# Kernel optimization log

Measured on AMD Instinct MI355X. Metric: run time of the kernel, lower is better.

## Reference

```python
import jax, jax.numpy as jnp
import numpy as np

B, C, H = 8, 512, 2048
GROUPS = 32
EPS = 1e-6


def setup_inputs() -> dict:
    key = jax.random.key(0)
    ks = jax.random.split(key, 10)
    s = 1.0 / np.sqrt(C)
    return {
        "x": jax.random.normal(ks[0], (B, C, H), dtype=jnp.float32),
        "gamma": jnp.ones((C,), jnp.float32),
        "beta": jnp.zeros((C,), jnp.float32),
        "wq": jax.random.normal(ks[1], (C, C), jnp.float32) * s,
        "bq": jnp.zeros((C,), jnp.float32),
        "wk": jax.random.normal(ks[2], (C, C), jnp.float32) * s,
        "bk": jnp.zeros((C,), jnp.float32),
        "wv": jax.random.normal(ks[3], (C, C), jnp.float32) * s,
        "bv": jnp.zeros((C,), jnp.float32),
        "wp": jax.random.normal(ks[4], (C, C), jnp.float32) * s,
        "bp": jnp.zeros((C,), jnp.float32),
    }


def group_norm(x, gamma, beta):
    b, c, h = x.shape
    xr = x.reshape(b, GROUPS, c // GROUPS, h)
    mean = xr.mean(axis=(2, 3), keepdims=True)
    var = xr.var(axis=(2, 3), keepdims=True)
    xn = ((xr - mean) * jax.lax.rsqrt(var + EPS)).reshape(b, c, h)
    return xn * gamma[None, :, None] + beta[None, :, None]


def conv1x1(x, w, b):
    # 1x1 Conv1d == channel-mixing GEMM: [C_out,C_in] x [b,C_in,h]
    return jnp.einsum("oc,bch->boh", w, x) + b[None, :, None]


def reference(x, gamma, beta, wq, bq, wk, bk, wv, bv, wp, bp):
    b, c, h = x.shape
    hn = group_norm(x, gamma, beta)
    q = conv1x1(hn, wq, bq)  # [b,c,h]
    k = conv1x1(hn, wk, bk)
    v = conv1x1(hn, wv, bv)
    # scores w[b,i,j] = sum_c q[b,c,i] k[b,c,j] / sqrt(c)
    w = jnp.einsum("bci,bcj->bij", q, k) * (c ** -0.5)
    w = jax.nn.softmax(w, axis=2)
    # h_[b,c,i] = sum_j v[b,c,j] w[b,i,j]
    h_ = jnp.einsum("bcj,bij->bci", v, w)
    out = conv1x1(h_, wp, bp)
    return x + out
```

## Files before the change

### kernel.cpp

```cpp
#include <hip/hip_runtime.h>
#include <stdint.h>

typedef unsigned short u16;
typedef short s16x8 __attribute__((ext_vector_type(8)));
typedef float f32x4 __attribute__((ext_vector_type(4)));

#define BM 128
#define BN 128
#define BK 32
#define KPAD 40

#define WAITV(n) asm volatile("s_waitcnt vmcnt(" #n ")" ::: "memory")
#define BARR()   asm volatile("s_barrier" ::: "memory")
#define SB0()    __builtin_amdgcn_sched_barrier(0)

__device__ __forceinline__ float bf2f(u16 b) {
    union { unsigned int u; float f; } v; v.u = ((unsigned int)b) << 16; return v.f;
}
__device__ __forceinline__ u16 f2bf(float f) {
    union { float f; unsigned int u; } v; v.f = f;
    unsigned int u = v.u;
    u += 0x7fffu + ((u >> 16) & 1u);
    return (u16)(u >> 16);
}
__device__ __forceinline__ void async_cp16(const u16* g, u16* l) {
    __builtin_amdgcn_global_load_lds((const __attribute__((address_space(1))) void*)g,
                                     (__attribute__((address_space(3))) void*)l, 16, 0, 0);
}

__global__ __launch_bounds__(256) void gn_stats(const float* __restrict__ x,
                                                float* __restrict__ mean,
                                                float* __restrict__ rstd) {
    const int bg = blockIdx.x;
    const float* p = x + (long)bg * 16 * 2048;
    float s = 0.f, ss = 0.f;
    for (int it = 0; it < 32; it++) {
        const float4 v = *reinterpret_cast<const float4*>(p + ((it * 256 + threadIdx.x) << 2));
        s += v.x + v.y + v.z + v.w;
        ss += v.x * v.x + v.y * v.y + v.z * v.z + v.w * v.w;
    }
    const int lane = threadIdx.x & 63, wave = threadIdx.x >> 6;
#pragma unroll
    for (int o = 32; o > 0; o >>= 1) { s += __shfl_down(s, o, 64); ss += __shfl_down(ss, o, 64); }
    __shared__ float rb[8];
    if (lane == 0) { rb[wave] = s; rb[4 + wave] = ss; }
    __syncthreads();
    if (threadIdx.x == 0) {
        float S = rb[0] + rb[1] + rb[2] + rb[3];
        float SS = rb[4] + rb[5] + rb[6] + rb[7];
        float mu = S * (1.f / 32768.f);
        float var = SS * (1.f / 32768.f) - mu * mu;
        mean[bg] = mu;
        rstd[bg] = rsqrtf(var + 1e-6f);
    }
}

__global__ __launch_bounds__(256) void gn_apply_t(const float* __restrict__ x,
                                                  const float* __restrict__ gamma,
                                                  const float* __restrict__ beta,
                                                  const float* __restrict__ mean,
                                                  const float* __restrict__ rstd,
                                                  u16* __restrict__ hnT) {
    const int b = blockIdx.z, c0 = blockIdx.y * 64, h0 = blockIdx.x * 64;
    __shared__ __align__(16) u16 T[64][72];
    const int tid = threadIdx.x;
#pragma unroll
    for (int sidx = 0; sidx < 4; sidx++) {
        int ch = tid + sidx * 256;
        int cc = ch >> 4, h4 = (ch & 15) * 4;
        int c = c0 + cc;
        float mu = mean[b * 32 + (c >> 4)], rs = rstd[b * 32 + (c >> 4)];
        float ga = gamma[c], be = beta[c];
        const float4 v = *reinterpret_cast<const float4*>(x + ((long)b * 512 + c) * 2048 + h0 + h4);
        ushort4 pk;
        pk.x = f2bf((v.x - mu) * rs * ga + be);
        pk.y = f2bf((v.y - mu) * rs * ga + be);
        pk.z = f2bf((v.z - mu) * rs * ga + be);
        pk.w = f2bf((v.w - mu) * rs * ga + be);
        *reinterpret_cast<ushort4*>(&T[cc][h4]) = pk;
    }
    __syncthreads();
#pragma unroll
    for (int sidx = 0; sidx < 2; sidx++) {
        int ch = tid + sidx * 256;
        int hh = ch >> 3, c8 = (ch & 7) * 8;
        unsigned int o[4];
#pragma unroll
        for (int i = 0; i < 4; i++) {
            u16 lo = T[c8 + 2 * i][hh];
            u16 hi = T[c8 + 2 * i + 1][hh];
            o[i] = (unsigned int)lo | ((unsigned int)hi << 16);
        }
        *reinterpret_cast<uint4*>(hnT + ((long)b * 2048 + h0 + hh) * 512 + c0 + c8) =
            uint4{o[0], o[1], o[2], o[3]};
    }
}

__global__ __launch_bounds__(256) void w2bf(const float* __restrict__ a,
                                            const float* __restrict__ b,
                                            const float* __restrict__ c,
                                            u16* __restrict__ dst) {
    const float* s = (blockIdx.y == 0) ? a : (blockIdx.y == 1) ? b : c;
    const int i = (blockIdx.x * 256 + threadIdx.x) * 4;
    const float4 v = *reinterpret_cast<const float4*>(s + i);
    ushort4 p;
    p.x = f2bf(v.x); p.y = f2bf(v.y); p.z = f2bf(v.z); p.w = f2bf(v.w);
    *reinterpret_cast<ushort4*>(dst + (long)blockIdx.y * 262144 + i) = p;
}

__global__ __launch_bounds__(256) void softmax_rows(u16* __restrict__ S) {
    u16* p = S + (long)blockIdx.x * 2048;
    const int tid = threadIdx.x;
    uint4 v = *reinterpret_cast<const uint4*>(p + (tid << 3));
    unsigned int w[4] = {v.x, v.y, v.z, v.w};
    float f[8];
#pragma unroll
    for (int i = 0; i < 4; i++) {
        f[2 * i]     = bf2f((u16)(w[i] & 0xffffu));
        f[2 * i + 1] = bf2f((u16)(w[i] >> 16));
    }
    float m = f[0];
#pragma unroll
    for (int i = 1; i < 8; i++) m = fmaxf(m, f[i]);
    const int lane = tid & 63, wave = tid >> 6;
#pragma unroll
    for (int o = 32; o > 0; o >>= 1) m = fmaxf(m, __shfl_down(m, o, 64));
    __shared__ float rb[4];
    __shared__ float bc;
    if (lane == 0) rb[wave] = m;
    __syncthreads();
    if (tid == 0) bc = fmaxf(fmaxf(rb[0], rb[1]), fmaxf(rb[2], rb[3]));
    __syncthreads();
    m = bc;
    float s = 0.f;
#pragma unroll
    for (int i = 0; i < 8; i++) { f[i] = __expf(f[i] - m); s += f[i]; }
#pragma unroll
    for (int o = 32; o > 0; o >>= 1) s += __shfl_down(s, o, 64);
    __syncthreads();
    if (lane == 0) rb[wave] = s;
    __syncthreads();
    if (tid == 0) bc = 1.f / (rb[0] + rb[1] + rb[2] + rb[3]);
    __syncthreads();
    const float inv = bc;
#pragma unroll
    for (int i = 0; i < 4; i++)
        w[i] = (unsigned int)f2bf(f[2 * i] * inv) | ((unsigned int)f2bf(f[2 * i + 1] * inv) << 16);
    *reinterpret_cast<uint4*>(p + (tid << 3)) = uint4{w[0], w[1], w[2], w[3]};
}

__global__ __launch_bounds__(512, 1) void gemm256_s(const u16* __restrict__ Ag, long sA,
                                                    const u16* __restrict__ Bg, long sB,
                                                    u16* __restrict__ Og, long sO,
                                                    int K, int lda, int ldb, int ldo,
                                                    float scale) {
    const int bx = blockIdx.x;
    const int b = bx & 7, s = bx >> 3;
    const int ty = s & 7, tx = s >> 3;
    const int m0 = ty * 256, n0 = tx * 256;
    Ag += (long)b * sA;
    Bg += (long)b * sB;
    u16* O = Og + (long)b * sO;

    __shared__ __align__(16) u16 LA[2][2][128 * 64];
    __shared__ __align__(16) u16 LB[2][2][128 * 64];

    const int tid = threadIdx.x;
    const int lane = tid & 63, wave = tid >> 6;
    const int wm = wave >> 2, w4 = wave & 3;
    const int l15 = lane & 15, quad = lane >> 4;

    const int qxu   = ((quad << 4) ^ ((lane & 4) << 3)) >> 1;
    const int arow_u = (wm * 64 + l15) * 64;
    const int brow_u = (w4 * 32 + l15) * 64;

    const int l8 = lane >> 3;
    const int lrow0 = wave * 8 + l8;
    const int sEl = (((lane & 7) ^ ((lane & 32) >> 4)) << 3);
    int pA[2], pB[2];
    pA[0] = (m0 + lrow0) * lda + sEl;
    pA[1] = (m0 + 64 + lrow0) * lda + sEl;
    {
        const int gb = (lrow0 >> 5) * 64 + (lrow0 & 31);
        pB[0] = (n0 + gb) * ldb + sEl;
        pB[1] = (n0 + gb + 32) * ldb + sEl;
    }
    const int jA = 128 * lda;
    const int jB = 128 * ldb;

    auto stageA = [&](int buf, int mh, int k0) {
        u16* d = &LA[buf][mh][wave * 512];
        async_cp16(Ag + pA[mh] + k0, d);
        async_cp16(Ag + pA[mh] + jA + k0, d + 4096);
    };
    auto stageB = [&](int buf, int nh, int k0) {
        u16* d = &LB[buf][nh][wave * 512];
        async_cp16(Bg + pB[nh] + k0, d);
        async_cp16(Bg + pB[nh] + jB + k0, d + 4096);
    };

    f32x4 acc[8][4];
#pragma unroll
    for (int i = 0; i < 8; i++)
#pragma unroll
        for (int j = 0; j < 4; j++) acc[i][j] = f32x4{0.f, 0.f, 0.f, 0.f};

    s16x8 fa[4][2], fblo[2][2], fbhi[2][2];

    const int NT = K >> 6;

    stageA(0, 0, 0);
    stageB(0, 0, 0);
    stageB(0, 1, 0);
    stageA(0, 1, 0);
    if (NT > 1) {
        stageA(1, 0, 64);
        stageB(1, 0, 64);
        stageB(1, 1, 64);
    }
    WAITV(8); SB0();
    BARR(); SB0();

    for (int t = 0; t < NT; t++) {
        const int buf = t & 1;
        const int k2 = (t + 2) << 6;
        {
            const u16* Ar = &LA[buf][0][0];
            const u16* Br = &LB[buf][0][0];
#pragma unroll
            for (int mf = 0; mf < 4; mf++)
#pragma unroll
                for (int ks = 0; ks < 2; ks++)
                    fa[mf][ks] = *reinterpret_cast<const s16x8*>(Ar + arow_u + mf * 1024 + ks * 32 + qxu);
#pragma unroll
            for (int nf = 0; nf < 2; nf++)
#pragma unroll
                for (int ks = 0; ks < 2; ks++)
                    fblo[nf][ks] = *reinterpret_cast<const s16x8*>(Br + brow_u + nf * 1024 + ks * 32 + qxu);
            if (t + 1 < NT) stageA(buf ^ 1, 1, (t + 1) << 6);
            if (t == NT - 1) { WAITV(2); } else { WAITV(8); }
            SB0();
            BARR(); SB0();
            __builtin_amdgcn_s_setprio(1);
#pragma unroll
            for (int mf = 0; mf < 4; mf++)
#pragma unroll
                for (int nf = 0; nf < 2; nf++)
#pragma unroll
                    for (int ks = 0; ks < 2; ks++)
                        acc[mf][nf] = __builtin_amdgcn_mfma_f32_16x16x32_bf16(fa[mf][ks], fblo[nf][ks], acc[mf][nf], 0, 0, 0);
            __builtin_amdgcn_s_setprio(0);
            BARR(); SB0();
        }
        {
            const u16* Br = &LB[buf][1][0];
#pragma unroll
            for (int nf = 0; nf < 2; nf++)
#pragma unroll
                for (int ks = 0; ks < 2; ks++)
                    fbhi[nf][ks] = *reinterpret_cast<const s16x8*>(Br + brow_u + nf * 1024 + ks * 32 + qxu);
            if (t + 2 < NT) stageA(buf, 0, k2);
            if (t == NT - 1) { WAITV(0); } else { WAITV(8); }
            SB0();
            BARR(); SB0();
            __builtin_amdgcn_s_setprio(1);
#pragma unroll
            for (int mf = 0; mf < 4; mf++)
#pragma unroll
                for (int nf = 0; nf < 2; nf++)
#pragma unroll
                    for (int ks = 0; ks < 2; ks++)
                        acc[mf][2 + nf] = __builtin_amdgcn_mfma_f32_16x16x32_bf16(fa[mf][ks], fbhi[nf][ks], acc[mf][2 + nf], 0, 0, 0);
            __builtin_amdgcn_s_setprio(0);
            BARR(); SB0();
        }
        {
            const u16* Ar = &LA[buf][1][0];
#pragma unroll
            for (int mf = 0; mf < 4; mf++)
#pragma unroll
                for (int ks = 0; ks < 2; ks++)
                    fa[mf][ks] = *reinterpret_cast<const s16x8*>(Ar + arow_u + mf * 1024 + ks * 32 + qxu);
            if (t + 2 < NT) stageB(buf, 0, k2);
            WAITV(8); SB0();
            BARR(); SB0();
            __builtin_amdgcn_s_setprio(1);
#pragma unroll
            for (int mf = 0; mf < 4; mf++)
#pragma unroll
                for (int nf = 0; nf < 2; nf++)
#pragma unroll
                    for (int ks = 0; ks < 2; ks++)
                        acc[4 + mf][2 + nf] = __builtin_amdgcn_mfma_f32_16x16x32_bf16(fa[mf][ks], fbhi[nf][ks], acc[4 + mf][2 + nf], 0, 0, 0);
            __builtin_amdgcn_s_setprio(0);
            BARR(); SB0();
        }
        {
            if (t + 2 < NT) stageB(buf, 1, k2);
            if (t == NT - 2) { WAITV(4); } else { WAITV(8); }
            SB0();
            BARR(); SB0();
            __builtin_amdgcn_s_setprio(1);
#pragma unroll
            for (int mf = 0; mf < 4; mf++)
#pragma unroll
                for (int nf = 0; nf < 2; nf++)
#pragma unroll
                    for (int ks = 0; ks < 2; ks++)
                        acc[4 + mf][nf] = __builtin_amdgcn_mfma_f32_16x16x32_bf16(fa[mf][ks], fblo[nf][ks], acc[4 + mf][nf], 0, 0, 0);
            __builtin_amdgcn_s_setprio(0);
            BARR(); SB0();
        }
    }

    const int orow = m0 + wm * 128 + quad * 4;
    const int ocol = n0 + w4 * 64 + l15;
#pragma unroll
    for (int mi = 0; mi < 8; mi++)
#pragma unroll
        for (int ni = 0; ni < 4; ni++) {
            const long rb = (long)(orow + mi * 16) * ldo + ocol + ni * 16;
#pragma unroll
            for (int r = 0; r < 4; r++)
                O[rb + (long)r * ldo] = f2bf(acc[mi][ni][r] * scale);
        }
}

template <int EPI, int SWIZ>
__global__ __launch_bounds__(256) void gemm_tn_a(const u16* __restrict__ Ag, long sA,
                                                 const u16* __restrict__ Bg, long sB,
                                                 const float* __restrict__ bias,
                                                 const float* __restrict__ Xg, long sX,
                                                 void* __restrict__ Ogv, long sO,
                                                 int K, int lda, int ldb, int ldo,
                                                 float scale) {
    const int b = blockIdx.z;
    Ag += (long)b * sA;
    Bg += (long)b * sB;
    int tx, ty;
    if (SWIZ == 1) {
        const int xcd = blockIdx.x & 7, s = blockIdx.x >> 3;
        ty = xcd + 8 * (s >> 2);
        tx = s & 3;
    } else if (SWIZ == 2) {
        const int xcd = blockIdx.x & 7, s = blockIdx.x >> 3;
        ty = (xcd & 3) * 4 + (s & 3);
        tx = (xcd >> 2) * 8 + (s >> 2);
    } else {
        tx = blockIdx.x; ty = blockIdx.y;
    }
    const int m0 = ty * BM;
    const int n0 = tx * BN;

    __shared__ __align__(16) u16 As[3][BM * BK];
    __shared__ __align__(16) u16 Bs[3][BN * BK];

    const int tid = threadIdx.x;
    const int wave = tid >> 6;
    const int lane = tid & 63;
    const int quad = lane >> 4;
    const int l16 = lane & 15;
    const int wm = (wave >> 1) * 64;
    const int wn = (wave & 1) * 64;
    const int rl = lane >> 2;
    const int cl = (lane & 3) * 8;

    f32x4 acc[4][4];
#pragma unroll
    for (int i = 0; i < 4; i++)
#pragma unroll
        for (int j = 0; j < 4; j++) acc[i][j] = f32x4{0.f, 0.f, 0.f, 0.f};

    auto stage = [&](int buf, int k0) {
#pragma unroll
        for (int j = 0; j < 2; j++) {
            const int rbase = wave * 32 + j * 16;
            async_cp16(Ag + (long)(m0 + rbase + rl) * lda + k0 + cl, &As[buf][rbase * BK]);
            async_cp16(Bg + (long)(n0 + rbase + rl) * ldb + k0 + cl, &Bs[buf][rbase * BK]);
        }
    };
    auto compute = [&](int buf) {
        s16x8 af[4], bfr[4];
#pragma unroll
        for (int i = 0; i < 4; i++)
            af[i] = *reinterpret_cast<const s16x8*>(&As[buf][(wm + i * 16 + l16) * BK + quad * 8]);
#pragma unroll
        for (int j = 0; j < 4; j++)
            bfr[j] = *reinterpret_cast<const s16x8*>(&Bs[buf][(wn + j * 16 + l16) * BK + quad * 8]);
#pragma unroll
        for (int i = 0; i < 4; i++)
#pragma unroll
            for (int j = 0; j < 4; j++)
                acc[i][j] = __builtin_amdgcn_mfma_f32_16x16x32_bf16(af[i], bfr[j], acc[i][j], 0, 0, 0);
    };

    const int nsteps = K / BK;
    stage(0, 0);
    stage(1, BK);
    int t = 0;
    for (; t < nsteps - 1; t++) {
        asm volatile("s_waitcnt vmcnt(4)" ::: "memory");
        asm volatile("s_barrier" ::: "memory");
        if (t + 2 < nsteps) stage((t + 2) % 3, (t + 2) * BK);
        compute(t % 3);
    }
    asm volatile("s_waitcnt vmcnt(0)" ::: "memory");
    asm volatile("s_barrier" ::: "memory");
    compute(t % 3);

#pragma unroll
    for (int i = 0; i < 4; i++) {
        const int mb = m0 + wm + i * 16 + quad * 4;
#pragma unroll
        for (int j = 0; j < 4; j++) {
            const int n = n0 + wn + j * 16 + l16;
            if (EPI == 0) {
                u16* O = (u16*)Ogv + (long)b * sO;
#pragma unroll
                for (int r = 0; r < 4; r++) {
                    float vv = acc[i][j][r] * scale;
                    if (bias) vv += bias[mb + r];
                    O[(long)(mb + r) * ldo + n] = f2bf(vv);
                }
            } else if (EPI == 1) {
                u16* O = (u16*)Ogv + (long)b * sO;
                ushort4 pk;
                pk.x = f2bf(acc[i][j][0] + bias[mb + 0]);
                pk.y = f2bf(acc[i][j][1] + bias[mb + 1]);
                pk.z = f2bf(acc[i][j][2] + bias[mb + 2]);
                pk.w = f2bf(acc[i][j][3] + bias[mb + 3]);
                *reinterpret_cast<ushort4*>(&O[(long)n * ldo + mb]) = pk;
            } else {
                float* O = (float*)Ogv + (long)b * sO;
                const float* X = Xg + (long)b * sX;
                const float bn = bias[n];
                const float4 xv = *reinterpret_cast<const float4*>(&X[(long)n * ldo + mb]);
                float4 pk;
                pk.x = acc[i][j][0] + bn + xv.x;
                pk.y = acc[i][j][1] + bn + xv.y;
                pk.z = acc[i][j][2] + bn + xv.z;
                pk.w = acc[i][j][3] + bn + xv.w;
                *reinterpret_cast<float4*>(&O[(long)n * ldo + mb]) = pk;
            }
        }
    }
}

__global__ __launch_bounds__(256) void qkv_a(const u16* __restrict__ wb3,
                                             const u16* __restrict__ hnT,
                                             const float* __restrict__ bq,
                                             const float* __restrict__ bk,
                                             const float* __restrict__ bv,
                                             u16* __restrict__ qT, u16* __restrict__ kT,
                                             u16* __restrict__ vv) {
    const long HC = 1048576;
    const int b = blockIdx.z;
    const int xcd = blockIdx.x & 7, s = blockIdx.x >> 3;
    const int hi = (s >= 12) ? 1 : 0;
    const int yy = s - hi * 12;
    const int x = xcd + 8 * hi;
    const int which = yy >> 2;
    const int my = yy & 3;
    const u16* Ag = wb3 + which * 262144;
    const u16* Bg = hnT + (long)b * HC;
    const int m0 = my * BM;
    const int n0 = x * BN;

    __shared__ __align__(16) u16 As[3][BM * BK];
    __shared__ __align__(16) u16 Bs[3][BN * BK];

    const int tid = threadIdx.x;
    const int wave = tid >> 6;
    const int lane = tid & 63;
    const int quad = lane >> 4;
    const int l16 = lane & 15;
    const int wm = (wave >> 1) * 64;
    const int wn = (wave & 1) * 64;
    const int rl = lane >> 2;
    const int cl = (lane & 3) * 8;

    f32x4 acc[4][4];
#pragma unroll
    for (int i = 0; i < 4; i++)
#pragma unroll
        for (int j = 0; j < 4; j++) acc[i][j] = f32x4{0.f, 0.f, 0.f, 0.f};

    auto stage = [&](int buf, int k0) {
#pragma unroll
        for (int j = 0; j < 2; j++) {
            const int rbase = wave * 32 + j * 16;
            async_cp16(Ag + (long)(m0 + rbase + rl) * 512 + k0 + cl, &As[buf][rbase * BK]);
            async_cp16(Bg + (long)(n0 + rbase + rl) * 512 + k0 + cl, &Bs[buf][rbase * BK]);
        }
    };
    auto compute = [&](int buf) {
        s16x8 af[4], bfr[4];
#pragma unroll
        for (int i = 0; i < 4; i++)
            af[i] = *reinterpret_cast<const s16x8*>(&As[buf][(wm + i * 16 + l16) * BK + quad * 8]);
#pragma unroll
        for (int j = 0; j < 4; j++)
            bfr[j] = *reinterpret_cast<const s16x8*>(&Bs[buf][(wn + j * 16 + l16) * BK + quad * 8]);
#pragma unroll
        for (int i = 0; i < 4; i++)
#pragma unroll
            for (int j = 0; j < 4; j++)
                acc[i][j] = __builtin_amdgcn_mfma_f32_16x16x32_bf16(af[i], bfr[j], acc[i][j], 0, 0, 0);
    };

    const int nsteps = 512 / BK;
    stage(0, 0);
    stage(1, BK);
    int t = 0;
    for (; t < nsteps - 1; t++) {
        asm volatile("s_waitcnt vmcnt(4)" ::: "memory");
        asm volatile("s_barrier" ::: "memory");
        if (t + 2 < nsteps) stage((t + 2) % 3, (t + 2) * BK);
        compute(t % 3);
    }
    asm volatile("s_waitcnt vmcnt(0)" ::: "memory");
    asm volatile("s_barrier" ::: "memory");
    compute(t % 3);

    if (which == 2) {
        u16* O = vv + (long)b * HC;
#pragma unroll
        for (int i = 0; i < 4; i++) {
            const int mb = m0 + wm + i * 16 + quad * 4;
#pragma unroll
            for (int j = 0; j < 4; j++) {
                const int n = n0 + wn + j * 16 + l16;
#pragma unroll
                for (int r = 0; r < 4; r++)
                    O[(long)(mb + r) * 2048 + n] = f2bf(acc[i][j][r] + bv[mb + r]);
            }
        }
    } else {
        const float* bias = which ? bk : bq;
        u16* O = (which ? kT : qT) + (long)b * HC;
#pragma unroll
        for (int i = 0; i < 4; i++) {
            const int mb = m0 + wm + i * 16 + quad * 4;
#pragma unroll
            for (int j = 0; j < 4; j++) {
                const int n = n0 + wn + j * 16 + l16;
                ushort4 pk;
                pk.x = f2bf(acc[i][j][0] + bias[mb + 0]);
                pk.y = f2bf(acc[i][j][1] + bias[mb + 1]);
                pk.z = f2bf(acc[i][j][2] + bias[mb + 2]);
                pk.w = f2bf(acc[i][j][3] + bias[mb + 3]);
                *reinterpret_cast<ushort4*>(&O[(long)n * 512 + mb]) = pk;
            }
        }
    }
}

template <int F32>
__device__ __forceinline__ void stage_tile(const char* G, int ld, int r0, int k0,
                                           u16* __restrict__ lds, int tid) {
    if (F32) {
        const float* g = (const float*)G;
#pragma unroll
        for (int s = 0; s < 4; s++) {
            const int c = tid + s * 256;
            const int row = c >> 3, col = (c & 7) * 4;
            const float4 v = *reinterpret_cast<const float4*>(g + (long)(r0 + row) * ld + k0 + col);
            ushort4 pk;
            pk.x = f2bf(v.x); pk.y = f2bf(v.y); pk.z = f2bf(v.z); pk.w = f2bf(v.w);
            *reinterpret_cast<ushort4*>(&lds[row * KPAD + col]) = pk;
        }
    } else {
        const u16* g = (const u16*)G;
#pragma unroll
        for (int s = 0; s < 2; s++) {
            const int c = tid + s * 256;
            const int row = c >> 2, col = (c & 3) * 8;
            const uint4 v = *reinterpret_cast<const uint4*>(g + (long)(r0 + row) * ld + k0 + col);
            *reinterpret_cast<uint4*>(&lds[row * KPAD + col]) = v;
        }
    }
}

template <int EPI, int AF32, int BF32>
__global__ __launch_bounds__(256) void gemm_tn(const void* __restrict__ Agv, long sA,
                                               const void* __restrict__ Bgv, long sB,
                                               const float* __restrict__ bias,
                                               const float* __restrict__ Xg, long sX,
                                               void* __restrict__ Ogv, long sO,
                                               int K, int lda, int ldb, int ldo,
                                               float scale) {
    const int b = blockIdx.z;
    const char* A8 = (const char*)Agv + (long)b * sA * (AF32 ? 4 : 2);
    const char* B8 = (const char*)Bgv + (long)b * sB * (BF32 ? 4 : 2);
    const int m0 = blockIdx.y * BM;
    const int n0 = blockIdx.x * BN;

    __shared__ __align__(16) u16 As[BM * KPAD];
    __shared__ __align__(16) u16 Bs[BN * KPAD];

    const int tid = threadIdx.x;
    const int wave = tid >> 6;
    const int lane = tid & 63;
    const int quad = lane >> 4;
    const int l16 = lane & 15;
    const int wm = (wave >> 1) * 64;
    const int wn = (wave & 1) * 64;

    f32x4 acc[4][4];
#pragma unroll
    for (int i = 0; i < 4; i++)
#pragma unroll
        for (int j = 0; j < 4; j++) acc[i][j] = f32x4{0.f, 0.f, 0.f, 0.f};

    for (int k0 = 0; k0 < K; k0 += BK) {
        __syncthreads();
        stage_tile<AF32>(A8, lda, m0, k0, As, tid);
        stage_tile<BF32>(B8, ldb, n0, k0, Bs, tid);
        __syncthreads();
        s16x8 af[4], bfr[4];
#pragma unroll
        for (int i = 0; i < 4; i++)
            af[i] = *reinterpret_cast<const s16x8*>(&As[(wm + i * 16 + l16) * KPAD + quad * 8]);
#pragma unroll
        for (int j = 0; j < 4; j++)
            bfr[j] = *reinterpret_cast<const s16x8*>(&Bs[(wn + j * 16 + l16) * KPAD + quad * 8]);
#pragma unroll
        for (int i = 0; i < 4; i++)
#pragma unroll
            for (int j = 0; j < 4; j++)
                acc[i][j] = __builtin_amdgcn_mfma_f32_16x16x32_bf16(af[i], bfr[j], acc[i][j], 0, 0, 0);
    }

#pragma unroll
    for (int i = 0; i < 4; i++) {
        const int mb = m0 + wm + i * 16 + quad * 4;
#pragma unroll
        for (int j = 0; j < 4; j++) {
            const int n = n0 + wn + j * 16 + l16;
            if (EPI == 0) {
                u16* O = (u16*)Ogv + (long)b * sO;
#pragma unroll
                for (int r = 0; r < 4; r++) {
                    float vv = acc[i][j][r] * scale;
                    if (bias) vv += bias[mb + r];
                    O[(long)(mb + r) * ldo + n] = f2bf(vv);
                }
            } else if (EPI == 1) {
                u16* O = (u16*)Ogv + (long)b * sO;
                ushort4 pk;
                pk.x = f2bf(acc[i][j][0] + bias[mb + 0]);
                pk.y = f2bf(acc[i][j][1] + bias[mb + 1]);
                pk.z = f2bf(acc[i][j][2] + bias[mb + 2]);
                pk.w = f2bf(acc[i][j][3] + bias[mb + 3]);
                *reinterpret_cast<ushort4*>(&O[(long)n * ldo + mb]) = pk;
            } else {
                float* O = (float*)Ogv + (long)b * sO;
                const float* X = Xg + (long)b * sX;
                const float bn = bias[n];
                const float4 xv = *reinterpret_cast<const float4*>(&X[(long)n * ldo + mb]);
                float4 pk;
                pk.x = acc[i][j][0] + bn + xv.x;
                pk.y = acc[i][j][1] + bn + xv.y;
                pk.z = acc[i][j][2] + bn + xv.z;
                pk.w = acc[i][j][3] + bn + xv.w;
                *reinterpret_cast<float4*>(&O[(long)n * ldo + mb]) = pk;
            }
        }
    }
}

extern "C" void kernel_launch(void* const* d_in, const int* in_sizes, int n_in,
                              void* d_out, int out_size, void* d_ws, size_t ws_size,
                              hipStream_t stream) {
    const float* x     = (const float*)d_in[0];
    const float* gamma = (const float*)d_in[1];
    const float* beta  = (const float*)d_in[2];
    const float* wq    = (const float*)d_in[3];
    const float* bq    = (const float*)d_in[4];
    const float* wk    = (const float*)d_in[5];
    const float* bk    = (const float*)d_in[6];
    const float* wv    = (const float*)d_in[7];
    const float* bv    = (const float*)d_in[8];
    const float* wp    = (const float*)d_in[9];
    const float* bp    = (const float*)d_in[10];
    float* out = (float*)d_out;

    const long HC = (long)2048 * 512;
    const long HH = (long)2048 * 2048;
    const long WSZ = 512 * 512;
    const float scl = 0.044194173824159216f;

    char* ws = (char*)d_ws;
    float* meanb = (float*)ws;
    float* rstdb = (float*)(ws + 1024);
    u16* base = (u16*)(ws + 4096);

    const size_t FULL_NEED   = 4096 + 2 * (size_t)(24 * HC + 8 * HH);
    const size_t MED_NEED    = 4096 + 2 * (size_t)(32 * HC + HH);
    const size_t SMALL_NEED  = 4096 + 2 * (size_t)(4 * HC + HH);
    const size_t CHUNK512    = 4096 + 2 * (size_t)(4 * HC + 512 * 2048);

    gn_stats<<<256, 256, 0, stream>>>(x, meanb, rstdb);

    if (ws_size >= FULL_NEED) {
        u16* qT  = base;
        u16* kT  = qT + 8 * HC;
        u16* vv  = kT + 8 * HC;
        u16* Sb  = vv + 8 * HC;
        u16* hnT = Sb;
        u16* wb3 = Sb + 8 * HH - 3 * WSZ;
        u16* hT  = qT;
        u16* wpb = vv;

        w2bf<<<dim3(256, 3), 256, 0, stream>>>(wq, wk, wv, wb3);
        gn_apply_t<<<dim3(32, 8, 8), 256, 0, stream>>>(x, gamma, beta, meanb, rstdb, hnT);
        qkv_a<<<dim3(192, 1, 8), 256, 0, stream>>>(wb3, hnT, bq, bk, bv, qT, kT, vv);
        gemm256_s<<<dim3(512), 512, 0, stream>>>(qT, HC, kT, HC, Sb, HH,
                                                 512, 512, 512, 2048, scl);
        softmax_rows<<<16384, 256, 0, stream>>>(Sb);
        gemm_tn_a<0, 1><<<dim3(64, 1, 8), 256, 0, stream>>>(Sb, HH, vv, HC, nullptr, nullptr, 0,
                                                            hT, HC, 2048, 2048, 2048, 512, 1.f);
        w2bf<<<dim3(256, 1), 256, 0, stream>>>(wp, wp, wp, wpb);
        gemm_tn_a<2, 1><<<dim3(64, 1, 8), 256, 0, stream>>>(hT, HC, wpb, 0, bp, x, HC,
                                                            out, HC, 512, 512, 512, 2048, 1.f);
    } else if (ws_size >= MED_NEED) {
        u16* hnT = base;
        u16* qT  = hnT + 8 * HC;
        u16* kT  = qT + 8 * HC;
        u16* vv  = kT + 8 * HC;
        u16* Sb  = vv + 8 * HC;
        u16* hT  = hnT;
        gn_apply_t<<<dim3(32, 8, 8), 256, 0, stream>>>(x, gamma, beta, meanb, rstdb, hnT);
        gemm_tn<1, 1, 0><<<dim3(16, 4, 8), 256, 0, stream>>>(wq, 0, hnT, HC, bq, nullptr, 0,
                                                             qT, HC, 512, 512, 512, 512, 1.f);
        gemm_tn<1, 1, 0><<<dim3(16, 4, 8), 256, 0, stream>>>(wk, 0, hnT, HC, bk, nullptr, 0,
                                                             kT, HC, 512, 512, 512, 512, 1.f);
        gemm_tn<0, 1, 0><<<dim3(16, 4, 8), 256, 0, stream>>>(wv, 0, hnT, HC, bv, nullptr, 0,
                                                             vv, HC, 512, 512, 512, 2048, 1.f);
        for (int b = 0; b < 8; b++) {
            gemm_tn<0, 0, 0><<<dim3(16, 16, 1), 256, 0, stream>>>(qT + b * HC, 0, kT + b * HC, 0,
                                                                  nullptr, nullptr, 0, Sb, 0,
                                                                  512, 512, 512, 2048, scl);
            softmax_rows<<<2048, 256, 0, stream>>>(Sb);
            gemm_tn<0, 0, 0><<<dim3(4, 16, 1), 256, 0, stream>>>(Sb, 0, vv + b * HC, 0,
                                                                 nullptr, nullptr, 0, hT + b * HC, 0,
                                                                 2048, 2048, 2048, 512, 1.f);
        }
        gemm_tn<2, 0, 1><<<dim3(4, 16, 8), 256, 0, stream>>>(hT, HC, wp, 0, bp, x, HC,
                                                             out, HC, 512, 512, 512, 2048, 1.f);
    } else {
        const int CH = (ws_size >= SMALL_NEED) ? 2048 : ((ws_size >= CHUNK512) ? 512 : 128);
        u16* hn = base;
        u16* q  = hn + HC;
        u16* k  = q + HC;
        u16* v  = k + HC;
        u16* Sc = v + HC;
        u16* hT = hn;
        for (int b = 0; b < 8; b++) {
            const float* xb = x + (long)b * HC;
            gn_apply_t<<<dim3(32, 8, 1), 256, 0, stream>>>(xb, gamma, beta,
                                                           meanb + b * 32, rstdb + b * 32, hn);
            gemm_tn<1, 1, 0><<<dim3(16, 4, 1), 256, 0, stream>>>(wq, 0, hn, 0, bq, nullptr, 0,
                                                                 q, 0, 512, 512, 512, 512, 1.f);
            gemm_tn<1, 1, 0><<<dim3(16, 4, 1), 256, 0, stream>>>(wk, 0, hn, 0, bk, nullptr, 0,
                                                                 k, 0, 512, 512, 512, 512, 1.f);
            gemm_tn<0, 1, 0><<<dim3(16, 4, 1), 256, 0, stream>>>(wv, 0, hn, 0, bv, nullptr, 0,
                                                                 v, 0, 512, 512, 512, 2048, 1.f);
            for (int i0 = 0; i0 < 2048; i0 += CH) {
                gemm_tn<0, 0, 0><<<dim3(16, CH / 128, 1), 256, 0, stream>>>(
                    q + (long)i0 * 512, 0, k, 0, nullptr, nullptr, 0, Sc, 0,
                    512, 512, 512, 2048, scl);
                softmax_rows<<<CH, 256, 0, stream>>>(Sc);
                gemm_tn<0, 0, 0><<<dim3(4, CH / 128, 1), 256, 0, stream>>>(
                    Sc, 0, v, 0, nullptr, nullptr, 0, hT + (long)i0 * 512, 0,
                    2048, 2048, 2048, 512, 1.f);
            }
            gemm_tn<2, 0, 1><<<dim3(4, 16, 1), 256, 0, stream>>>(hT, 0, wp, 0, bp, xb, 0,
                                                                 out + (long)b * HC, 0,
                                                                 512, 512, 512, 2048, 1.f);
        }
    }
}
```

Baseline: 302.1 us.

## Add dedicated 256x128 pipelined GEMM kernel for attention-times-V product

Replaces the generic gemm_tn_a launch for the P·V product with a new 512-thread kernel using 256x128 output tiles, double-buffered LDS with async copies split into four compute phases, and swizzled LDS reads. The grid becomes 256 blocks over batch, 8 M tiles and 4 N tiles. The goal is better MFMA utilisation and load/compute overlap on the K=2048 reduction, though fewer blocks than CUs may leave some compute units idle.

```diff
diff --git a/kernel.cpp b/kernel.cpp
--- a/kernel.cpp
+++ b/kernel.cpp
@@ -317,6 +317,167 @@
     const int ocol = n0 + w4 * 64 + l15;
 #pragma unroll
     for (int mi = 0; mi < 8; mi++)
+#pragma unroll
+        for (int ni = 0; ni < 4; ni++) {
+            const long rb = (long)(orow + mi * 16) * ldo + ocol + ni * 16;
+#pragma unroll
+            for (int r = 0; r < 4; r++)
+                O[rb + (long)r * ldo] = f2bf(acc[mi][ni][r] * scale);
+        }
+}
+
+template <int EPI>
+__global__ __launch_bounds__(512, 1) void gemm256_pv(const u16* __restrict__ Ag, long sA,
+                                                     const u16* __restrict__ Bg, long sB,
+                                                     u16* __restrict__ Og, long sO,
+                                                     int K, int lda, int ldb, int ldo,
+                                                     float scale) {
+    const int bx = blockIdx.x;
+    const int b = bx & 7, s = bx >> 3;
+    const int mt = s >> 2, nt = s & 3;
+    const int m0 = mt * 256, n0 = nt * 128;
+    Ag += (long)b * sA;
+    Bg += (long)b * sB;
+    u16* O = Og + (long)b * sO;
+
+    __shared__ __align__(16) u16 LA[2][2][128 * 64];
+    __shared__ __align__(16) u16 LB[2][2][64 * 64];
+
+    const int tid = threadIdx.x;
+    const int lane = tid & 63, wave = tid >> 6;
+    const int wm = wave >> 1, wn = wave & 1;
+    const int l15 = lane & 15, quad = lane >> 4;
+
+    const int qxu = ((quad << 4) ^ ((lane & 4) << 3)) >> 1;
+
+    const int r0 = tid >> 3;
+    const int sEl = (((lane & 7) ^ ((lane & 32) >> 4)) << 3);
+    const int gA = (r0 >> 5) * 64 + (r0 & 31);
+    int pA[2], pB[2];
+    pA[0] = (m0 + gA) * lda + sEl;
+    pA[1] = (m0 + gA + 32) * lda + sEl;
+    pB[0] = (n0 + gA) * ldb + sEl;
+    pB[1] = (n0 + gA + 32) * ldb + sEl;
+    const int jA = 128 * lda;
+
+    auto stageA = [&](int buf, int mh, int k0) {
+        u16* d = &LA[buf][mh][wave * 512];
+        async_cp16(Ag + pA[mh] + k0, d);
+        async_cp16(Ag + pA[mh] + jA + k0, d + 4096);
+    };
+    auto stageBB = [&](int buf, int k0) {
+        async_cp16(Bg + pB[0] + k0, &LB[buf][0][wave * 512]);
+        async_cp16(Bg + pB[1] + k0, &LB[buf][1][wave * 512]);
+    };
+
+    f32x4 acc[4][4];
+#pragma unroll
+    for (int i = 0; i < 4; i++)
+#pragma unroll
+        for (int j = 0; j < 4; j++) acc[i][j] = f32x4{0.f, 0.f, 0.f, 0.f};
+
+    s16x8 fa[2][2], fblo[2][2], fbhi[2][2];
+
+    const int arow_u = (wm * 32 + l15) * 64;
+    const int brow_u = (wn * 32 + l15) * 64;
+
+    const int NT = K >> 6;
+
+    stageBB(0, 0);
+    stageA(0, 0, 0);
+    stageA(0, 1, 0);
+    if (NT > 1) stageBB(1, 64);
+    WAITV(4); SB0();
+    BARR(); SB0();
+
+    for (int t = 0; t < NT; t++) {
+        const int buf = t & 1;
+        const int k1 = (t + 1) << 6, k2 = (t + 2) << 6;
+        {
+            const u16* Ar = &LA[buf][0][0];
+            const u16* Br = &LB[buf][0][0];
+#pragma unroll
+            for (int mf = 0; mf < 2; mf++)
+#pragma unroll
+                for (int ks = 0; ks < 2; ks++)
+                    fa[mf][ks] = *reinterpret_cast<const s16x8*>(Ar + arow_u + mf * 1024 + ks * 32 + qxu);
+#pragma unroll
+            for (int nf = 0; nf < 2; nf++)
+#pragma unroll
+                for (int ks = 0; ks < 2; ks++)
+                    fblo[nf][ks] = *reinterpret_cast<const s16x8*>(Br + brow_u + nf * 1024 + ks * 32 + qxu);
+            if (t + 1 < NT) stageA(buf ^ 1, 0, k1);
+            __builtin_amdgcn_s_setprio(1);
+#pragma unroll
+            for (int mf = 0; mf < 2; mf++)
+#pragma unroll
+                for (int nf = 0; nf < 2; nf++)
+#pragma unroll
+                    for (int ks = 0; ks < 2; ks++)
+                        acc[mf][nf] = __builtin_amdgcn_mfma_f32_16x16x32_bf16(fa[mf][ks], fblo[nf][ks], acc[mf][nf], 0, 0, 0);
+            __builtin_amdgcn_s_setprio(0);
+            if (t == NT - 1) { WAITV(0); } else { WAITV(4); }
+            SB0();
+            BARR(); SB0();
+        }
+        {
+            const u16* Br = &LB[buf][1][0];
+#pragma unroll
+            for (int nf = 0; nf < 2; nf++)
+#pragma unroll
+                for (int ks = 0; ks < 2; ks++)
+                    fbhi[nf][ks] = *reinterpret_cast<const s16x8*>(Br + brow_u + nf * 1024 + ks * 32 + qxu);
+            if (t + 1 < NT) stageA(buf ^ 1, 1, k1);
+            __builtin_amdgcn_s_setprio(1);
+#pragma unroll
+            for (int mf = 0; mf < 2; mf++)
+#pragma unroll
+                for (int nf = 0; nf < 2; nf++)
+#pragma unroll
+                    for (int ks = 0; ks < 2; ks++)
+                        acc[mf][2 + nf] = __builtin_amdgcn_mfma_f32_16x16x32_bf16(fa[mf][ks], fbhi[nf][ks], acc[mf][2 + nf], 0, 0, 0);
+            __builtin_amdgcn_s_setprio(0);
+            BARR(); SB0();
+        }
+        {
+            const u16* Ar = &LA[buf][1][0];
+#pragma unroll
+            for (int mf = 0; mf < 2; mf++)
+#pragma unroll
+                for (int ks = 0; ks < 2; ks++)
+                    fa[mf][ks] = *reinterpret_cast<const s16x8*>(Ar + arow_u + mf * 1024 + ks * 32 + qxu);
+            if (t + 2 < NT) stageBB(buf, k2);
+            __builtin_amdgcn_s_setprio(1);
+#pragma unroll
+            for (int mf = 0; mf < 2; mf++)
+#pragma unroll
+                for (int nf = 0; nf < 2; nf++)
+#pragma unroll
+                    for (int ks = 0; ks < 2; ks++)
+                        acc[2 + mf][2 + nf] = __builtin_amdgcn_mfma_f32_16x16x32_bf16(fa[mf][ks], fbhi[nf][ks], acc[2 + mf][2 + nf], 0, 0, 0);
+            __builtin_amdgcn_s_setprio(0);
+            BARR(); SB0();
+        }
+        {
+            __builtin_amdgcn_s_setprio(1);
+#pragma unroll
+            for (int mf = 0; mf < 2; mf++)
+#pragma unroll
+                for (int nf = 0; nf < 2; nf++)
+#pragma unroll
+                    for (int ks = 0; ks < 2; ks++)
+                        acc[2 + mf][nf] = __builtin_amdgcn_mfma_f32_16x16x32_bf16(fa[mf][ks], fblo[nf][ks], acc[2 + mf][nf], 0, 0, 0);
+            __builtin_amdgcn_s_setprio(0);
+            if (t == NT - 2) { WAITV(2); } else if (t < NT - 2) { WAITV(4); }
+            SB0();
+            BARR(); SB0();
+        }
+    }
+
+    const int orow = m0 + wm * 64 + quad * 4;
+    const int ocol = n0 + wn * 64 + l15;
+#pragma unroll
+    for (int mi = 0; mi < 4; mi++)
 #pragma unroll
         for (int ni = 0; ni < 4; ni++) {
             const long rb = (long)(orow + mi * 16) * ldo + ocol + ni * 16;
@@ -718,8 +879,8 @@
         gemm256_s<<<dim3(512), 512, 0, stream>>>(qT, HC, kT, HC, Sb, HH,
                                                  512, 512, 512, 2048, scl);
         softmax_rows<<<16384, 256, 0, stream>>>(Sb);
-        gemm_tn_a<0, 1><<<dim3(64, 1, 8), 256, 0, stream>>>(Sb, HH, vv, HC, nullptr, nullptr, 0,
-                                                            hT, HC, 2048, 2048, 2048, 512, 1.f);
+        gemm256_pv<0><<<dim3(256), 512, 0, stream>>>(Sb, HH, vv, HC, hT, HC,
+                                                     2048, 2048, 2048, 512, 1.f);
         w2bf<<<dim3(256, 1), 256, 0, stream>>>(wp, wp, wp, wpb);
         gemm_tn_a<2, 1><<<dim3(64, 1, 8), 256, 0, stream>>>(hT, HC, wpb, 0, bp, x, HC,
                                                             out, HC, 512, 512, 512, 2048, 1.f);
```

Result: faster. 291.6 us (-3.5%).
